# Performance work log

Hardware: AMD Instinct MI355X
Metric: run time of the kernel (lower is better)

## Reference

```python
import jax, jax.numpy as jnp
import numpy as np

TARGET_H, TARGET_W = 602, 602
EPS = 1e-8
A = -0.75  # PyTorch bicubic kernel coefficient


def _cubic_kernel(x):
    # Keys cubic convolution kernel with a = -0.75 (PyTorch's choice), x >= 0
    x = np.abs(x)
    w = np.where(
        x <= 1.0,
        (A + 2.0) * x**3 - (A + 3.0) * x**2 + 1.0,
        np.where(x < 2.0, A * (x**3 - 5.0 * x**2 + 8.0 * x - 4.0), 0.0),
    )
    return w


def build_bicubic_matrix(in_size, out_size):
    # Row-stochastic [out_size, in_size] matrix equivalent to 1D bicubic resize
    # with align_corners=False and border replication (PyTorch F.interpolate).
    scale = in_size / out_size
    i = np.arange(out_size, dtype=np.float64)
    src = (i + 0.5) * scale - 0.5
    base = np.floor(src).astype(np.int64)
    t = src - base
    W = np.zeros((out_size, in_size), dtype=np.float64)
    for tap in range(-1, 3):
        idx = np.clip(base + tap, 0, in_size - 1)
        w = _cubic_kernel(t - tap)
        np.add.at(W, (np.arange(out_size), idx), w)
    return jnp.asarray(W, dtype=jnp.float32)


def setup_inputs() -> dict:
    key = jax.random.key(0)
    k1, k2 = jax.random.split(key)
    B, K, D, N = 4, 1849, 1024, 80
    feats = jax.random.normal(k1, (B, K, D), dtype=jnp.float32)
    embeddings = jax.random.normal(k2, (N, D), dtype=jnp.float32)
    return {"feats": feats, "embeddings": embeddings}


def reference(feats, embeddings) -> jnp.ndarray:
    B, K, D = feats.shape
    N = embeddings.shape[0]
    P = int(np.sqrt(K))  # patch grid side (43)

    # Cosine similarity ('init' branch with normalize=True), expressed as a GEMM
    dot = jnp.einsum("bkd,nd->bnk", feats, embeddings)  # [B,N,K]
    f_norm = jnp.linalg.norm(feats, axis=-1)       # [B,K]
    e_norm = jnp.linalg.norm(embeddings, axis=-1)  # [N]
    cosim = dot / (f_norm[:, None, :] * e_norm[None, :, None] + EPS)

    cosim = cosim.reshape(B, N, P, P)

    # Separable bicubic resize to (TARGET_H, TARGET_W)
    Wh = build_bicubic_matrix(P, TARGET_H)  # [602, P]
    Ww = build_bicubic_matrix(P, TARGET_W)  # [602, P]
    out = jnp.einsum("bnhw,Hh->bnHw", cosim, Wh)
    out = jnp.einsum("bnHw,Ww->bnHW", out, Ww)
    return out
```

## Files before the change

kernel.cpp:

```cpp
#include <hip/hip_runtime.h>
#include <math.h>

#define EPS 1e-8f
constexpr int D     = 1024;
constexpr int NEMB  = 80;
constexpr int K     = 1849;
constexpr int BATCH = 4;
constexpr int P     = 43;
constexpr int TGT   = 602;
constexpr int ROWS  = BATCH * K;
constexpr size_t PLANE = (size_t)BATCH * NEMB * K;
constexpr int SPLIT = 8;
constexpr int KC    = D / SPLIT;

__device__ inline double cubic_w(double x) {
  const double A = -0.75;
  x = fabs(x);
  if (x <= 1.0) return ((A + 2.0) * x - (A + 3.0)) * x * x + 1.0;
  if (x < 2.0)  return A * (((x - 5.0) * x + 8.0) * x - 4.0);
  return 0.0;
}

__device__ inline float block_reduce_sum256(float v) {
  #pragma unroll
  for (int off = 32; off > 0; off >>= 1) v += __shfl_down(v, off, 64);
  __shared__ float red[4];
  int lane = threadIdx.x & 63, wid = threadIdx.x >> 6;
  if (lane == 0) red[wid] = v;
  __syncthreads();
  float r = 0.f;
  if (threadIdx.x == 0) r = red[0] + red[1] + red[2] + red[3];
  return r;
}

__global__ __launch_bounds__(256) void prep_kernel(
    const float* __restrict__ emb, float* __restrict__ e_norm,
    float4* __restrict__ gtw) {
  int bid = blockIdx.x;
  if (bid < NEMB) {
    float4 v = ((const float4*)(emb + (size_t)bid * D))[threadIdx.x];
    float s = v.x * v.x + v.y * v.y + v.z * v.z + v.w * v.w;
    s = block_reduce_sum256(s);
    if (threadIdx.x == 0) e_norm[bid] = sqrtf(s);
  } else {
    int j = threadIdx.x;
    if (j < 14) {
      double scale = (double)P / (double)TGT;
      double src = ((double)j + 0.5) * scale - 0.5;
      double fb = floor(src);
      double t = src - fb;
      float4 w;
      w.x = (float)cubic_w(t + 1.0);
      w.y = (float)cubic_w(t);
      w.z = (float)cubic_w(t - 1.0);
      w.w = (float)cubic_w(t - 2.0);
      gtw[j] = w;
    }
  }
}

constexpr int BM  = 64;
constexpr int BK  = 32;
constexpr int LDA = 36;

__global__ __launch_bounds__(256) void gemm_partial(
    const float* __restrict__ feats, const float* __restrict__ emb,
    float* __restrict__ part, float* __restrict__ fpart) {
  __shared__ float As[BM * LDA];
  __shared__ float Bs[NEMB * LDA];
  int t = threadIdx.x;
  int row0 = blockIdx.x * BM;
  int s = blockIdx.y;
  int tr = t >> 4, tc = t & 15;
  float acc[4][5] = {{0.f}};
  float ssq0 = 0.f, ssq1 = 0.f;

  int kbeg = s * KC, kend = kbeg + KC;
  for (int k0 = kbeg; k0 < kend; k0 += BK) {
    int r = t >> 3, dg = t & 7;
    {
      int gr = row0 + r;
      float4 v = make_float4(0.f, 0.f, 0.f, 0.f);
      if (gr < ROWS) v = *(const float4*)(feats + (size_t)gr * D + k0 + dg * 4);
      ssq0 += v.x * v.x + v.y * v.y + v.z * v.z + v.w * v.w;
      *(float4*)(As + r * LDA + dg * 4) = v;
    }
    {
      int gr = row0 + 32 + r;
      float4 v = make_float4(0.f, 0.f, 0.f, 0.f);
      if (gr < ROWS) v = *(const float4*)(feats + (size_t)gr * D + k0 + dg * 4);
      ssq1 += v.x * v.x + v.y * v.y + v.z * v.z + v.w * v.w;
      *(float4*)(As + (32 + r) * LDA + dg * 4) = v;
    }
    #pragma unroll
    for (int it = 0; it < 3; ++it) {
      int i = t + it * 256;
      if (i < NEMB * 8) {
        int rb = i >> 3, dgb = i & 7;
        float4 v = *(const float4*)(emb + (size_t)rb * D + k0 + dgb * 4);
        *(float4*)(Bs + rb * LDA + dgb * 4) = v;
      }
    }
    __syncthreads();
    #pragma unroll
    for (int dd = 0; dd < BK; dd += 4) {
      float4 a[4], b[5];
      #pragma unroll
      for (int j = 0; j < 4; ++j)  a[j]  = *(const float4*)(As + (tr * 4 + j) * LDA + dd);
      #pragma unroll
      for (int i2 = 0; i2 < 5; ++i2) b[i2] = *(const float4*)(Bs + (tc + i2 * 16) * LDA + dd);
      #pragma unroll
      for (int j = 0; j < 4; ++j)
        #pragma unroll
        for (int i2 = 0; i2 < 5; ++i2)
          acc[j][i2] += a[j].x * b[i2].x + a[j].y * b[i2].y +
                        a[j].z * b[i2].z + a[j].w * b[i2].w;
    }
    __syncthreads();
  }

  #pragma unroll
  for (int off = 4; off > 0; off >>= 1) {
    ssq0 += __shfl_down(ssq0, off, 8);
    ssq1 += __shfl_down(ssq1, off, 8);
  }
  if ((t & 7) == 0) {
    int r = t >> 3;
    int gr0 = row0 + r, gr1 = row0 + 32 + r;
    if (gr0 < ROWS) fpart[(size_t)s * ROWS + gr0] = ssq0;
    if (gr1 < ROWS) fpart[(size_t)s * ROWS + gr1] = ssq1;
  }

  float* pplane = part + (size_t)s * PLANE;
  #pragma unroll
  for (int j = 0; j < 4; ++j) {
    int gr = row0 + tr * 4 + j;
    if (gr >= ROWS) continue;
    int b_ = gr / K;
    int k  = gr - b_ * K;
    #pragma unroll
    for (int i2 = 0; i2 < 5; ++i2) {
      int n = tc + i2 * 16;
      pplane[((size_t)(b_ * NEMB + n)) * K + k] = acc[j][i2];
    }
  }
}

__global__ __launch_bounds__(256) void reduce_kernel(
    const float* __restrict__ part, const float* __restrict__ fpart,
    const float* __restrict__ e_norm, float* __restrict__ cosim) {
  size_t e = (size_t)blockIdx.x * 256 + threadIdx.x;
  if (e >= PLANE) return;
  int bn = (int)(e / K);
  int k  = (int)(e - (size_t)bn * K);
  int b_ = bn / NEMB;
  int n  = bn - b_ * NEMB;
  int gr = b_ * K + k;
  float dot = 0.f, fn2 = 0.f;
  #pragma unroll
  for (int s = 0; s < SPLIT; ++s) {
    dot += part[(size_t)s * PLANE + e];
    fn2 += fpart[(size_t)s * ROWS + gr];
  }
  cosim[e] = dot / (sqrtf(fn2) * e_norm[n] + EPS);
}

__global__ __launch_bounds__(256) void resize_kernel(
    const float* __restrict__ cosim, const float4* __restrict__ gtw,
    float* __restrict__ out) {
  __shared__ float img[5 * P];
  __shared__ float tmp[5 * TGT];
  __shared__ float4 wq[14];
  __shared__ int4 ro[14];

  int bn = blockIdx.y;
  int c  = blockIdx.x;
  int t  = threadIdx.x;

  int hmin = max(0, c - 2), hmax = min(P - 1, c + 2);
  int NH = hmax - hmin + 1;

  if (t < 14) {
    wq[t] = gtw[t];
    int hb = c - 2 + (t >= 7);
    int4 o;
    o.x = min(P - 1, max(0, hb))     - hmin;
    o.y = min(P - 1, max(0, hb + 1)) - hmin;
    o.z = min(P - 1, max(0, hb + 2)) - hmin;
    o.w = min(P - 1, max(0, hb + 3)) - hmin;
    ro[t] = o;
  }
  const float* src = cosim + (size_t)bn * (P * P) + hmin * P;
  for (int i = t; i < NH * P; i += 256) img[i] = src[i];
  __syncthreads();

  for (int i = t; i < NH * TGT; i += 256) {
    int h = i / TGT;
    int W = i - h * TGT;
    int m = W / 14;
    int j = W - m * 14;
    int wb = m - 2 + (j >= 7);
    float4 w = wq[j];
    const float* rowp = img + h * P;
    int i0 = min(P - 1, max(0, wb));
    int i1 = min(P - 1, max(0, wb + 1));
    int i2 = min(P - 1, max(0, wb + 2));
    int i3 = min(P - 1, max(0, wb + 3));
    tmp[i] = w.x * rowp[i0] + w.y * rowp[i1] +
             w.z * rowp[i2] + w.w * rowp[i3];
  }
  __syncthreads();

  int H0 = c * 14;
  float* obase = out + (size_t)bn * TGT * TGT;
  constexpr int PAIRS = TGT / 2;
  for (int i = t; i < 14 * PAIRS; i += 256) {
    int r  = i / PAIRS;
    int pw = i - r * PAIRS;
    float4 hw = wq[r];
    int4 o = ro[r];
    const float* b0 = tmp + pw * 2;
    float2 a0 = *(const float2*)(b0 + o.x * TGT);
    float2 a1 = *(const float2*)(b0 + o.y * TGT);
    float2 a2 = *(const float2*)(b0 + o.z * TGT);
    float2 a3 = *(const float2*)(b0 + o.w * TGT);
    float2 ov;
    ov.x = hw.x * a0.x + hw.y * a1.x + hw.z * a2.x + hw.w * a3.x;
    ov.y = hw.x * a0.y + hw.y * a1.y + hw.z * a2.y + hw.w * a3.y;
    *(float2*)(obase + (size_t)(H0 + r) * TGT + pw * 2) = ov;
  }
}

extern "C" void kernel_launch(void* const* d_in, const int* in_sizes, int n_in,
                              void* d_out, int out_size, void* d_ws, size_t ws_size,
                              hipStream_t stream) {
  const float* feats = (const float*)d_in[0];
  const float* emb   = (const float*)d_in[1];
  float* out = (float*)d_out;
  char* ws = (char*)d_ws;

  auto align64 = [](size_t x) { return (x + 63) & ~(size_t)63; };
  size_t off = 0;
  float* cosim  = (float*)(ws + off); off = align64(off + PLANE * 4);
  float* e_norm = (float*)(ws + off); off = align64(off + NEMB * 4);
  float4* gtw   = (float4*)(ws + off); off = align64(off + 14 * 16);

  float* part  = (float*)d_out;
  float* fpart = part + (size_t)SPLIT * PLANE;

  prep_kernel<<<dim3(NEMB + 1), dim3(256), 0, stream>>>(emb, e_norm, gtw);
  gemm_partial<<<dim3((ROWS + BM - 1) / BM, SPLIT), dim3(256), 0, stream>>>(
      feats, emb, part, fpart);
  reduce_kernel<<<dim3((int)((PLANE + 255) / 256)), dim3(256), 0, stream>>>(
      part, fpart, e_norm, cosim);
  resize_kernel<<<dim3(43, 320), dim3(256), 0, stream>>>(cosim, gtw, out);
}
```

Measured before the change: 187.1 us.

## Fuse both resize passes into registers, one thread per output column pair

The resize kernel no longer stages horizontally-resized rows in shared memory. Each thread now computes the horizontal pass for its two output columns across the 5 source rows and keeps them in registers. It then applies the vertical weights directly, using compile-time row index patterns for the border blocks. This removes the tmp buffer, a barrier and the index divisions. Block size grows to 320 so that one thread covers each column pair, which leaves 19 threads idle per block.

```diff
diff --git a/kernel.cpp b/kernel.cpp
--- a/kernel.cpp
+++ b/kernel.cpp
@@ -165,13 +165,11 @@
   cosim[e] = dot / (sqrtf(fn2) * e_norm[n] + EPS);
 }
 
-__global__ __launch_bounds__(256) void resize_kernel(
+__global__ __launch_bounds__(320) void resize_kernel(
     const float* __restrict__ cosim, const float4* __restrict__ gtw,
     float* __restrict__ out) {
   __shared__ float img[5 * P];
-  __shared__ float tmp[5 * TGT];
   __shared__ float4 wq[14];
-  __shared__ int4 ro[14];
 
   int bn = blockIdx.y;
   int c  = blockIdx.x;
@@ -180,55 +178,69 @@
   int hmin = max(0, c - 2), hmax = min(P - 1, c + 2);
   int NH = hmax - hmin + 1;
 
-  if (t < 14) {
-    wq[t] = gtw[t];
-    int hb = c - 2 + (t >= 7);
-    int4 o;
-    o.x = min(P - 1, max(0, hb))     - hmin;
-    o.y = min(P - 1, max(0, hb + 1)) - hmin;
-    o.z = min(P - 1, max(0, hb + 2)) - hmin;
-    o.w = min(P - 1, max(0, hb + 3)) - hmin;
-    ro[t] = o;
-  }
+  if (t < 14) wq[t] = gtw[t];
   const float* src = cosim + (size_t)bn * (P * P) + hmin * P;
-  for (int i = t; i < NH * P; i += 256) img[i] = src[i];
+  for (int i = t; i < NH * P; i += 320) img[i] = src[i];
   __syncthreads();
 
-  for (int i = t; i < NH * TGT; i += 256) {
-    int h = i / TGT;
-    int W = i - h * TGT;
-    int m = W / 14;
-    int j = W - m * 14;
-    int wb = m - 2 + (j >= 7);
-    float4 w = wq[j];
+  int pw = t;
+  if (pw >= TGT / 2) return;
+
+  int W0 = pw * 2;
+  int m0 = W0 / 14;
+  int j0 = W0 - m0 * 14;
+  int wb0 = m0 - 2 + (j0 >= 7);
+  int j1 = (j0 == 13) ? 0 : j0 + 1;
+  int d  = (j0 == 6) ? 1 : 0;
+  float4 w0 = wq[j0], w1 = wq[j1];
+
+  int i0 = min(P - 1, max(0, wb0));
+  int i1 = min(P - 1, max(0, wb0 + 1));
+  int i2 = min(P - 1, max(0, wb0 + 2));
+  int i3 = min(P - 1, max(0, wb0 + 3));
+  int i4 = min(P - 1, max(0, wb0 + 4));
+
+  float ta[5], tb[5];
+  #pragma unroll
+  for (int h = 0; h < 5; ++h) {
     const float* rowp = img + h * P;
-    int i0 = min(P - 1, max(0, wb));
-    int i1 = min(P - 1, max(0, wb + 1));
-    int i2 = min(P - 1, max(0, wb + 2));
-    int i3 = min(P - 1, max(0, wb + 3));
-    tmp[i] = w.x * rowp[i0] + w.y * rowp[i1] +
-             w.z * rowp[i2] + w.w * rowp[i3];
-  }
-  __syncthreads();
-
-  int H0 = c * 14;
-  float* obase = out + (size_t)bn * TGT * TGT;
-  constexpr int PAIRS = TGT / 2;
-  for (int i = t; i < 14 * PAIRS; i += 256) {
-    int r  = i / PAIRS;
-    int pw = i - r * PAIRS;
-    float4 hw = wq[r];
-    int4 o = ro[r];
-    const float* b0 = tmp + pw * 2;
-    float2 a0 = *(const float2*)(b0 + o.x * TGT);
-    float2 a1 = *(const float2*)(b0 + o.y * TGT);
-    float2 a2 = *(const float2*)(b0 + o.z * TGT);
-    float2 a3 = *(const float2*)(b0 + o.w * TGT);
-    float2 ov;
-    ov.x = hw.x * a0.x + hw.y * a1.x + hw.z * a2.x + hw.w * a3.x;
-    ov.y = hw.x * a0.y + hw.y * a1.y + hw.z * a2.y + hw.w * a3.y;
-    *(float2*)(obase + (size_t)(H0 + r) * TGT + pw * 2) = ov;
-  }
+    float v0 = rowp[i0], v1 = rowp[i1], v2 = rowp[i2], v3 = rowp[i3], v4 = rowp[i4];
+    ta[h] = w0.x * v0 + w0.y * v1 + w0.z * v2 + w0.w * v3;
+    float u0 = d ? v1 : v0;
+    float u1 = d ? v2 : v1;
+    float u2 = d ? v3 : v2;
+    float u3 = d ? v4 : v3;
+    tb[h] = w1.x * u0 + w1.y * u1 + w1.z * u2 + w1.w * u3;
+  }
+
+  float* op = out + (size_t)bn * TGT * TGT + (size_t)(c * 14) * TGT + W0;
+
+  #define ROWS7(R0, a0, a1, a2, a3)                                        \
+    _Pragma("unroll")                                                      \
+    for (int r = R0; r < R0 + 7; ++r) {                                    \
+      float4 hw = wq[r];                                                   \
+      float ox = hw.x * ta[a0] + hw.y * ta[a1] + hw.z * ta[a2] + hw.w * ta[a3]; \
+      float oy = hw.x * tb[a0] + hw.y * tb[a1] + hw.z * tb[a2] + hw.w * tb[a3]; \
+      *(float2*)(op + (size_t)r * TGT) = make_float2(ox, oy);              \
+    }
+
+  if (c >= 2 && c <= 40) {
+    ROWS7(0, 0, 1, 2, 3)
+    ROWS7(7, 1, 2, 3, 4)
+  } else if (c == 0) {
+    ROWS7(0, 0, 0, 0, 1)
+    ROWS7(7, 0, 0, 1, 2)
+  } else if (c == 1) {
+    ROWS7(0, 0, 0, 1, 2)
+    ROWS7(7, 0, 1, 2, 3)
+  } else if (c == 41) {
+    ROWS7(0, 0, 1, 2, 3)
+    ROWS7(7, 1, 2, 3, 3)
+  } else {
+    ROWS7(0, 0, 1, 2, 2)
+    ROWS7(7, 1, 2, 2, 2)
+  }
+  #undef ROWS7
 }
 
 extern "C" void kernel_launch(void* const* d_in, const int* in_sizes, int n_in,
@@ -253,5 +265,5 @@
       feats, emb, part, fpart);
   reduce_kernel<<<dim3((int)((PLANE + 255) / 256)), dim3(256), 0, stream>>>(
       part, fpart, e_norm, cosim);
-  resize_kernel<<<dim3(43, 320), dim3(256), 0, stream>>>(cosim, gtw, out);
-}
+  resize_kernel<<<dim3(43, 320), dim3(320), 0, stream>>>(cosim, gtw, out);
+}
```

Measured after the change: 184.7 us. About the same (-1.3%).
